# Performance work log

Measured on AMD Instinct MI355X. Metric: run time of the kernel, lower is better.

The kernel has to match this reference:

```python
import jax, jax.numpy as jnp
import numpy as np

D_MODEL = 1024
NUM_HEADS = 16
D_K = D_MODEL // NUM_HEADS
SCALE = float(np.sqrt(D_K))


def setup_inputs() -> dict:
    key = jax.random.key(0)
    ks = jax.random.split(key, 11)
    B, S, D = 4, 2048, D_MODEL
    w_std = 1.0 / np.sqrt(D)
    inp = {
        "query": jax.random.normal(ks[0], (B, S, D), jnp.float32),
        "key": jax.random.normal(ks[1], (B, S, D), jnp.float32),
        "value": jax.random.normal(ks[2], (B, S, D), jnp.float32),
        "wq": jax.random.normal(ks[3], (D, D), jnp.float32) * w_std,
        "bq": jax.random.normal(ks[4], (D,), jnp.float32) * w_std,
        "wk": jax.random.normal(ks[5], (D, D), jnp.float32) * w_std,
        "bk": jax.random.normal(ks[6], (D,), jnp.float32) * w_std,
        "wv": jax.random.normal(ks[7], (D, D), jnp.float32) * w_std,
        "bv": jax.random.normal(ks[8], (D,), jnp.float32) * w_std,
        "wo": jax.random.normal(ks[9], (D, D), jnp.float32) * w_std,
        "bo": jax.random.normal(ks[10], (D,), jnp.float32) * w_std,
    }
    return inp


def reference(query, key, value, wq, bq, wk, bk, wv, bv, wo, bo):
    B, Sq, D = query.shape
    H, dk = NUM_HEADS, D_K
    # linear projections (weights stored as [in, out])
    q = query @ wq + bq
    k = key @ wk + bk
    v = value @ wv + bv
    # [B, H, S, d_k]
    q = q.reshape(B, Sq, H, dk).transpose(0, 2, 1, 3)
    k = k.reshape(B, -1, H, dk).transpose(0, 2, 1, 3)
    v = v.reshape(B, -1, H, dk).transpose(0, 2, 1, 3)
    # full attention scores [B, H, Sq, Sk]
    att = jnp.einsum("bhqd,bhkd->bhqk", q, k) / SCALE
    att = jax.nn.softmax(att, axis=-1)
    out = jnp.einsum("bhqk,bhkd->bhqd", att, v)
    out = out.transpose(0, 2, 1, 3).reshape(B, Sq, D)
    return out @ wo + bo
```

## Files before the change

kernel.cpp:

```cpp
#include <hip/hip_runtime.h>


typedef _Float16 fp16;
typedef fp16  fp16x8 __attribute__((ext_vector_type(8)));
typedef fp16  fp16x4 __attribute__((ext_vector_type(4)));
typedef __fp16 h16x2 __attribute__((ext_vector_type(2)));
typedef float f32x4  __attribute__((ext_vector_type(4)));

#define NROWS 8192
#define DM    1024
#define SEQ   2048
#define DK    64
#define LOG2E 1.44269504088896340736f
#define QSCALE (0.125f * LOG2E)

__device__ __forceinline__ f32x4 mfma16x16(fp16x8 a, fp16x8 b, f32x4 c) {
    return __builtin_amdgcn_mfma_f32_16x16x32_f16(a, b, c, 0, 0, 0);
}

__device__ __forceinline__ void gload16(const void* g, void* l) {
    __builtin_amdgcn_global_load_lds(
        (const __attribute__((address_space(1))) void*)g,
        (__attribute__((address_space(3))) void*)l, 16, 0, 0);
}

__device__ __forceinline__ fp16x8 cvt8(f32x4 a, f32x4 b) {
    h16x2 r0 = __builtin_amdgcn_cvt_pkrtz(a[0], a[1]);
    h16x2 r1 = __builtin_amdgcn_cvt_pkrtz(a[2], a[3]);
    h16x2 r2 = __builtin_amdgcn_cvt_pkrtz(b[0], b[1]);
    h16x2 r3 = __builtin_amdgcn_cvt_pkrtz(b[2], b[3]);
    fp16x8 v;
    v[0] = (fp16)r0[0]; v[1] = (fp16)r0[1]; v[2] = (fp16)r1[0]; v[3] = (fp16)r1[1];
    v[4] = (fp16)r2[0]; v[5] = (fp16)r2[1]; v[6] = (fp16)r3[0]; v[7] = (fp16)r3[1];
    return v;
}

__global__ __launch_bounds__(256) void transpose_w_kernel(
    const float* __restrict__ w0, const float* __restrict__ w1,
    const float* __restrict__ w2, const float* __restrict__ w3,
    fp16* __restrict__ t0, fp16* __restrict__ t1,
    fp16* __restrict__ t2, fp16* __restrict__ t3) {
    const int z = blockIdx.z;
    const float* W = (z == 0) ? w0 : (z == 1) ? w1 : (z == 2) ? w2 : w3;
    fp16*       T = (z == 0) ? t0 : (z == 1) ? t1 : (z == 2) ? t2 : t3;
    __shared__ float tile[32][33];
    const int tx = threadIdx.x, ty = threadIdx.y;
    const int bx = blockIdx.x * 32, by = blockIdx.y * 32;
#pragma unroll
    for (int j = 0; j < 4; ++j)
        tile[ty + 8 * j][tx] = W[(size_t)(by + ty + 8 * j) * DM + bx + tx];
    __syncthreads();
#pragma unroll
    for (int j = 0; j < 4; ++j)
        T[(size_t)(bx + ty + 8 * j) * DM + by + tx] = (fp16)tile[tx][ty + 8 * j];
}

__global__ __launch_bounds__(256) void gemm_qkv_kernel(
    const float* __restrict__ Xq, const float* __restrict__ Xk,
    const float* __restrict__ Xv,
    const fp16* __restrict__ Wq, const fp16* __restrict__ Wk,
    const fp16* __restrict__ Wv,
    const float* __restrict__ bq, const float* __restrict__ bk,
    const float* __restrict__ bv,
    fp16* __restrict__ Qb, fp16* __restrict__ Kb, fp16* __restrict__ Vtg) {
    const int i = blockIdx.x;
    const int xcd = i & 7, r = i >> 3;
    const int z = r >> 6, rr = r & 63;
    const int m0 = (xcd * 8 + (rr >> 3)) * 128;
    const int n0 = (rr & 7) * 128;

    const float* __restrict__ A = (z == 0) ? Xq : (z == 1) ? Xk : Xv;
    const fp16* __restrict__ B = (z == 0) ? Wq : (z == 1) ? Wk : Wv;
    const float* __restrict__ bias = (z == 0) ? bq : (z == 1) ? bk : bv;
    fp16* __restrict__ outp = (z == 0) ? Qb : (z == 1) ? Kb : Vtg;
    const float oscale = (z == 0) ? QSCALE : 1.0f;

    const int tid = threadIdx.x;
    const int lane = tid & 63;
    const int w = tid >> 6;
    const int wr = w >> 1, wc = w & 1;
    const int li = lane & 15, lg = lane >> 4;
    const int lrow8 = lane >> 3;
    const int lch8  = (lane & 7) ^ lrow8;
    const int lrow4 = lane >> 4;
    const int lch16 = (lane & 15);

    __shared__ float Atf[128 * 64];
    __shared__ fp16  Bt[128 * 64];

    f32x4 acc[4][4] = {};

    for (int k0 = 0; k0 < DM; k0 += 64) {
        __syncthreads();
#pragma unroll
        for (int it = 0; it < 8; ++it) {
            int R = (w * 8 + it) * 4 + lrow4;
            gload16(&A[(size_t)(m0 + R) * DM + k0 + ((lch16 ^ (R & 15)) * 4)],
                    &Atf[(w * 8 + it) * 256]);
        }
#pragma unroll
        for (int it = 0; it < 4; ++it) {
            int R = (w * 4 + it) * 8 + lrow8;
            gload16(&B[(size_t)(n0 + R) * DM + k0 + lch8 * 8], &Bt[(w * 4 + it) * 512]);
        }
        __syncthreads();
        fp16x8 af[4][2], bfr[4][2];
#pragma unroll
        for (int mf = 0; mf < 4; ++mf)
#pragma unroll
            for (int ks = 0; ks < 2; ++ks) {
                int R = wr * 64 + mf * 16 + li;
                int g0 = ks * 8 + lg * 2;
                f32x4 a0 = *(const f32x4*)&Atf[R * 64 + ((g0 ^ li) * 4)];
                f32x4 a1 = *(const f32x4*)&Atf[R * 64 + (((g0 + 1) ^ li) * 4)];
                af[mf][ks] = cvt8(a0, a1);
            }
#pragma unroll
        for (int nf = 0; nf < 4; ++nf)
#pragma unroll
            for (int ks = 0; ks < 2; ++ks)
                bfr[nf][ks] = *(const fp16x8*)&Bt[(wc * 64 + nf * 16 + li) * 64 +
                                                  (((ks * 4 + lg) ^ (li & 7)) * 8)];
#pragma unroll
        for (int ks = 0; ks < 2; ++ks)
#pragma unroll
            for (int mf = 0; mf < 4; ++mf)
#pragma unroll
                for (int nf = 0; nf < 4; ++nf)
                    acc[mf][nf] = mfma16x16(af[mf][ks], bfr[nf][ks], acc[mf][nf]);
    }
#pragma unroll
    for (int nf = 0; nf < 4; ++nf) {
        int col = n0 + wc * 64 + nf * 16 + li;
        float bv_ = bias[col];
        if (z == 2) {
#pragma unroll
            for (int mf = 0; mf < 4; ++mf) {
                int rowb = m0 + wr * 64 + mf * 16 + lg * 4;
                fp16x4 pk;
#pragma unroll
                for (int r2 = 0; r2 < 4; ++r2)
                    pk[r2] = (fp16)(acc[mf][nf][r2] + bv_);
                size_t o = ((size_t)(rowb >> 11) * 1024 + col) * SEQ + (rowb & 2047);
                *(fp16x4*)&outp[o] = pk;
            }
        } else {
#pragma unroll
            for (int mf = 0; mf < 4; ++mf)
#pragma unroll
                for (int r2 = 0; r2 < 4; ++r2) {
                    int row = m0 + wr * 64 + mf * 16 + lg * 4 + r2;
                    outp[(size_t)row * DM + col] = (fp16)((acc[mf][nf][r2] + bv_) * oscale);
                }
        }
    }
}

__global__ __launch_bounds__(256) void gemm_out_kernel(
    const fp16* __restrict__ A, const fp16* __restrict__ B,
    const float* __restrict__ bias, float* __restrict__ outp) {
    const int i = blockIdx.x;
    const int xcd = i & 7, r = i >> 3;
    const int m0 = (xcd * 8 + (r >> 4)) * 128;
    const int n0 = (r & 15) * 64;

    const int tid = threadIdx.x;
    const int lane = tid & 63;
    const int w = tid >> 6;
    const int wr = w >> 1, wc = w & 1;
    const int li = lane & 15, lg = lane >> 4;
    const int lrow = lane >> 3;
    const int lch  = (lane & 7) ^ lrow;

    __shared__ fp16 At[128 * 64];
    __shared__ fp16 Bt[64 * 64];

    f32x4 acc[4][2] = {};

    for (int k0 = 0; k0 < DM; k0 += 64) {
        __syncthreads();
#pragma unroll
        for (int it = 0; it < 4; ++it) {
            int R = (w * 4 + it) * 8 + lrow;
            gload16(&A[(size_t)(m0 + R) * DM + k0 + lch * 8], &At[(w * 4 + it) * 512]);
            if (it < 2) {
                int Rb = (w * 2 + it) * 8 + lrow;
                gload16(&B[(size_t)(n0 + Rb) * DM + k0 + lch * 8], &Bt[(w * 2 + it) * 512]);
            }
        }
        __syncthreads();
        fp16x8 af[4][2], bfr[2][2];
#pragma unroll
        for (int mf = 0; mf < 4; ++mf)
#pragma unroll
            for (int ks = 0; ks < 2; ++ks)
                af[mf][ks] = *(const fp16x8*)&At[(wr * 64 + mf * 16 + li) * 64 +
                                                 (((ks * 4 + lg) ^ (li & 7)) * 8)];
#pragma unroll
        for (int nf = 0; nf < 2; ++nf)
#pragma unroll
            for (int ks = 0; ks < 2; ++ks)
                bfr[nf][ks] = *(const fp16x8*)&Bt[(wc * 32 + nf * 16 + li) * 64 +
                                                  (((ks * 4 + lg) ^ (li & 7)) * 8)];
#pragma unroll
        for (int ks = 0; ks < 2; ++ks)
#pragma unroll
            for (int mf = 0; mf < 4; ++mf)
#pragma unroll
                for (int nf = 0; nf < 2; ++nf)
                    acc[mf][nf] = mfma16x16(af[mf][ks], bfr[nf][ks], acc[mf][nf]);
    }
#pragma unroll
    for (int nf = 0; nf < 2; ++nf) {
        int col = n0 + wc * 32 + nf * 16 + li;
        float bv_ = bias[col];
#pragma unroll
        for (int mf = 0; mf < 4; ++mf)
#pragma unroll
            for (int r2 = 0; r2 < 4; ++r2) {
                int row = m0 + wr * 64 + mf * 16 + lg * 4 + r2;
                outp[(size_t)row * DM + col] = acc[mf][nf][r2] + bv_;
            }
    }
}

__global__ __launch_bounds__(512) void attn_kernel(
    const fp16* __restrict__ Qb, const fp16* __restrict__ Kb,
    const fp16* __restrict__ Vtg, fp16* __restrict__ Of) {
    const int tid = threadIdx.x;
    const int lane = tid & 63;
    const int w = tid >> 6;
    const int li = lane & 15, lg = lane >> 4;

    int L = blockIdx.x;
    L = (L & 7) * 64 + (L >> 3);
    const int qt = L & 7, bh = L >> 3;
    const int b = bh >> 4, h = bh & 15;
    const size_t rowQ = (size_t)b * SEQ + (size_t)qt * 256;
    const int c0 = h * DK;

    __shared__ fp16 Kt[2][64 * 64];
    __shared__ fp16 Vt[2][64 * 64];
    __shared__ fp16 Pl[8][32 * 64];

    fp16x8 qf[2][2];
#pragma unroll
    for (int mf = 0; mf < 2; ++mf)
#pragma unroll
        for (int ks = 0; ks < 2; ++ks)
            qf[mf][ks] = *(const fp16x8*)&Qb[(rowQ + w * 32 + mf * 16 + li) * DM +
                                             c0 + ks * 32 + lg * 8];

    fp16x8 ones;
#pragma unroll
    for (int j = 0; j < 8; ++j) ones[j] = (fp16)1.0f;

    f32x4 oacc[2][4] = {};
    f32x4 lacc[2] = {};

    const int sr = tid >> 3, sc = tid & 7;
    const int ssl = sc ^ (sr & 7);
    fp16x8 rk, rv;
    rk = *(const fp16x8*)&Kb[((size_t)b * SEQ + sr) * DM + c0 + sc * 8];
    rv = *(const fp16x8*)&Vtg[((size_t)bh * 64 + sr) * SEQ + sc * 8];
    *(fp16x8*)&Kt[0][sr * 64 + ssl * 8] = rk;
    *(fp16x8*)&Vt[0][sr * 64 + ssl * 8] = rv;
    __syncthreads();

    for (int kt = 0; kt < SEQ / 64; ++kt) {
        const int cur = kt & 1;
        const bool more = (kt + 1 < SEQ / 64);
        if (more) {
            rk = *(const fp16x8*)&Kb[((size_t)b * SEQ + (kt + 1) * 64 + sr) * DM + c0 + sc * 8];
            rv = *(const fp16x8*)&Vtg[((size_t)bh * 64 + sr) * SEQ + (kt + 1) * 64 + sc * 8];
        }

        f32x4 s[4][2] = {};
        __builtin_amdgcn_s_setprio(1);
#pragma unroll
        for (int nf = 0; nf < 4; ++nf)
#pragma unroll
            for (int ks = 0; ks < 2; ++ks) {
                fp16x8 kf = *(const fp16x8*)&Kt[cur][(nf * 16 + li) * 64 +
                                                     (((ks * 4 + lg) ^ (li & 7)) * 8)];
#pragma unroll
                for (int mf = 0; mf < 2; ++mf)
                    s[nf][mf] = mfma16x16(kf, qf[mf][ks], s[nf][mf]);
            }
        __builtin_amdgcn_s_setprio(0);

#pragma unroll
        for (int mf = 0; mf < 2; ++mf) {
            fp16x4 pk[4];
#pragma unroll
            for (int nf = 0; nf < 4; ++nf)
#pragma unroll
                for (int r = 0; r < 4; ++r)
                    pk[nf][r] = (fp16)__builtin_amdgcn_exp2f(s[nf][mf][r]);
            int row = mf * 16 + li;
#pragma unroll
            for (int nf = 0; nf < 4; ++nf) {
                int sl = (nf * 2 + (lg >> 1)) ^ (li & 7);
                *(fp16x4*)&Pl[w][row * 64 + sl * 8 + (lg & 1) * 4] = pk[nf];
            }
        }

        __builtin_amdgcn_s_setprio(1);
#pragma unroll
        for (int ks = 0; ks < 2; ++ks) {
            fp16x8 pf[2];
#pragma unroll
            for (int mf = 0; mf < 2; ++mf) {
                pf[mf] = *(const fp16x8*)&Pl[w][(mf * 16 + li) * 64 +
                                                (((ks * 4 + lg) ^ (li & 7)) * 8)];
                lacc[mf] = mfma16x16(pf[mf], ones, lacc[mf]);
            }
#pragma unroll
            for (int nf = 0; nf < 4; ++nf) {
                fp16x8 vf = *(const fp16x8*)&Vt[cur][(nf * 16 + li) * 64 +
                                                     (((ks * 4 + lg) ^ (li & 7)) * 8)];
#pragma unroll
                for (int mf = 0; mf < 2; ++mf)
                    oacc[mf][nf] = mfma16x16(pf[mf], vf, oacc[mf][nf]);
            }
        }
        __builtin_amdgcn_s_setprio(0);

        if (more) {
            *(fp16x8*)&Kt[cur ^ 1][sr * 64 + ssl * 8] = rk;
            *(fp16x8*)&Vt[cur ^ 1][sr * 64 + ssl * 8] = rv;
            __syncthreads();
        }
    }

#pragma unroll
    for (int mf = 0; mf < 2; ++mf) {
#pragma unroll
        for (int r = 0; r < 4; ++r) {
            float linv = 1.0f / lacc[mf][r];
            size_t row = rowQ + w * 32 + mf * 16 + lg * 4 + r;
#pragma unroll
            for (int nf = 0; nf < 4; ++nf) {
                int col = c0 + nf * 16 + li;
                Of[row * DM + col] = (fp16)(oacc[mf][nf][r] * linv);
            }
        }
    }
}

extern "C" void kernel_launch(void* const* d_in, const int* in_sizes, int n_in,
                              void* d_out, int out_size, void* d_ws, size_t ws_size,
                              hipStream_t stream) {
    const float* query = (const float*)d_in[0];
    const float* key   = (const float*)d_in[1];
    const float* value = (const float*)d_in[2];
    const float* wq    = (const float*)d_in[3];
    const float* bq    = (const float*)d_in[4];
    const float* wk    = (const float*)d_in[5];
    const float* bk    = (const float*)d_in[6];
    const float* wv    = (const float*)d_in[7];
    const float* bv    = (const float*)d_in[8];
    const float* wo    = (const float*)d_in[9];
    const float* bo    = (const float*)d_in[10];

    char* ws = (char*)d_ws;
    const size_t SZX = (size_t)NROWS * DM * 2;
    const size_t SZW = (size_t)DM * DM * 2;
    fp16* Wtq = (fp16*)(ws);
    fp16* Wtk = (fp16*)(ws + SZW);
    fp16* Wtv = (fp16*)(ws + 2 * SZW);
    fp16* Wto = (fp16*)(ws + 3 * SZW);
    fp16* Qb  = (fp16*)(ws + 4 * SZW);
    fp16* Kb  = (fp16*)(ws + 4 * SZW + SZX);
    fp16* Vtg = (fp16*)(ws + 4 * SZW + 2 * SZX);
    fp16* Of  = (fp16*)(ws + 4 * SZW + 3 * SZX);

    const dim3 bT(32, 8);

    transpose_w_kernel<<<dim3(32, 32, 4), bT, 0, stream>>>(
        wq, wk, wv, wo, Wtq, Wtk, Wtv, Wto);
    gemm_qkv_kernel<<<1536, 256, 0, stream>>>(
        query, key, value, Wtq, Wtk, Wtv, bq, bk, bv, Qb, Kb, Vtg);
    attn_kernel<<<512, 512, 0, stream>>>(Qb, Kb, Vtg, Of);
    gemm_out_kernel<<<1024, 256, 0, stream>>>(Of, Wto, bo, (float*)d_out);
}
```

Measured before the change: 192.2 us.

## Prefetch A into registers and double-buffer B tiles in QKV projection GEMM

The QKV projection GEMM no longer stages fp32 activations through LDS. Each lane loads its A fragments straight from global memory into registers one k-step ahead. The fp16 weight tile is double-buffered in LDS, so the next tile's global→LDS load is issued while the current one is consumed, which drops one barrier per k-iteration. MFMA issue is wrapped in s_setprio to favour the math waves. The cost is more registers for the prefetched A values, and per-lane global loads that are less coalesced than the previous staged layout.

```diff
diff --git a/kernel.cpp b/kernel.cpp
--- a/kernel.cpp
+++ b/kernel.cpp
@@ -82,45 +82,61 @@
     const int li = lane & 15, lg = lane >> 4;
     const int lrow8 = lane >> 3;
     const int lch8  = (lane & 7) ^ lrow8;
-    const int lrow4 = lane >> 4;
-    const int lch16 = (lane & 15);
-
-    __shared__ float Atf[128 * 64];
-    __shared__ fp16  Bt[128 * 64];
+
+    __shared__ fp16 Bt[2][128 * 64];
 
     f32x4 acc[4][4] = {};
+    f32x4 areg[4][2][2];
+
+    const float* Abase = &A[(size_t)(m0 + wr * 64 + li) * DM + lg * 8];
+
+#pragma unroll
+    for (int it = 0; it < 4; ++it) {
+        int R = (w * 4 + it) * 8 + lrow8;
+        gload16(&B[(size_t)(n0 + R) * DM + lch8 * 8], &Bt[0][(w * 4 + it) * 512]);
+    }
+#pragma unroll
+    for (int mf = 0; mf < 4; ++mf)
+#pragma unroll
+        for (int ks = 0; ks < 2; ++ks) {
+            areg[mf][ks][0] = *(const f32x4*)&Abase[(size_t)mf * 16 * DM + ks * 32];
+            areg[mf][ks][1] = *(const f32x4*)&Abase[(size_t)mf * 16 * DM + ks * 32 + 4];
+        }
 
     for (int k0 = 0; k0 < DM; k0 += 64) {
+        const int cur = (k0 >> 6) & 1;
         __syncthreads();
-#pragma unroll
-        for (int it = 0; it < 8; ++it) {
-            int R = (w * 8 + it) * 4 + lrow4;
-            gload16(&A[(size_t)(m0 + R) * DM + k0 + ((lch16 ^ (R & 15)) * 4)],
-                    &Atf[(w * 8 + it) * 256]);
-        }
-#pragma unroll
-        for (int it = 0; it < 4; ++it) {
-            int R = (w * 4 + it) * 8 + lrow8;
-            gload16(&B[(size_t)(n0 + R) * DM + k0 + lch8 * 8], &Bt[(w * 4 + it) * 512]);
-        }
-        __syncthreads();
-        fp16x8 af[4][2], bfr[4][2];
+        if (k0 + 64 < DM) {
+#pragma unroll
+            for (int it = 0; it < 4; ++it) {
+                int R = (w * 4 + it) * 8 + lrow8;
+                gload16(&B[(size_t)(n0 + R) * DM + k0 + 64 + lch8 * 8],
+                        &Bt[cur ^ 1][(w * 4 + it) * 512]);
+            }
+        }
+        fp16x8 af[4][2];
 #pragma unroll
         for (int mf = 0; mf < 4; ++mf)
 #pragma unroll
-            for (int ks = 0; ks < 2; ++ks) {
-                int R = wr * 64 + mf * 16 + li;
-                int g0 = ks * 8 + lg * 2;
-                f32x4 a0 = *(const f32x4*)&Atf[R * 64 + ((g0 ^ li) * 4)];
-                f32x4 a1 = *(const f32x4*)&Atf[R * 64 + (((g0 + 1) ^ li) * 4)];
-                af[mf][ks] = cvt8(a0, a1);
-            }
+            for (int ks = 0; ks < 2; ++ks)
+                af[mf][ks] = cvt8(areg[mf][ks][0], areg[mf][ks][1]);
+        if (k0 + 64 < DM) {
+#pragma unroll
+            for (int mf = 0; mf < 4; ++mf)
+#pragma unroll
+                for (int ks = 0; ks < 2; ++ks) {
+                    areg[mf][ks][0] = *(const f32x4*)&Abase[(size_t)mf * 16 * DM + k0 + 64 + ks * 32];
+                    areg[mf][ks][1] = *(const f32x4*)&Abase[(size_t)mf * 16 * DM + k0 + 64 + ks * 32 + 4];
+                }
+        }
+        fp16x8 bfr[4][2];
 #pragma unroll
         for (int nf = 0; nf < 4; ++nf)
 #pragma unroll
             for (int ks = 0; ks < 2; ++ks)
-                bfr[nf][ks] = *(const fp16x8*)&Bt[(wc * 64 + nf * 16 + li) * 64 +
-                                                  (((ks * 4 + lg) ^ (li & 7)) * 8)];
+                bfr[nf][ks] = *(const fp16x8*)&Bt[cur][(wc * 64 + nf * 16 + li) * 64 +
+                                                       (((ks * 4 + lg) ^ (li & 7)) * 8)];
+        __builtin_amdgcn_s_setprio(1);
 #pragma unroll
         for (int ks = 0; ks < 2; ++ks)
 #pragma unroll
@@ -128,6 +144,7 @@
 #pragma unroll
                 for (int nf = 0; nf < 4; ++nf)
                     acc[mf][nf] = mfma16x16(af[mf][ks], bfr[nf][ks], acc[mf][nf]);
+        __builtin_amdgcn_s_setprio(0);
     }
 #pragma unroll
     for (int nf = 0; nf < 4; ++nf) {
```

Result: slower. 318.6 us (+65.7%).
